# Performance work log

Measured on AMD Instinct MI355X. Metric: run time of the kernel, lower is better.

The kernel has to match this reference:

```python
import jax, jax.numpy as jnp
import numpy as np


def _l2norm(x, axis):
    # F.normalize: x / max(||x||_2, eps)
    n = jnp.sqrt(jnp.sum(x * x, axis=axis, keepdims=True))
    return x / jnp.maximum(n, 1e-12)


def setup_inputs() -> dict:
    key = jax.random.key(0)
    k1, k2 = jax.random.split(key)
    B, N, H = 32768, 2048, 512
    z = jax.random.normal(k1, (B, H), dtype=jnp.float32)
    memory_items = jax.random.normal(k2, (N, H), dtype=jnp.float32)
    return {"z": z, "memory_items": memory_items}


def reference(z, memory_items):
    # ---- read path: cosine-similarity attention over memory bank ----
    z_n = _l2norm(z, axis=1)                     # (B,H)
    m_n = _l2norm(memory_items, axis=1)          # (N,H)
    similarity = z_n @ m_n.T                     # (B,N)
    weights = jax.nn.softmax(similarity, axis=1)  # (B,N)
    z_hat = weights @ memory_items               # (B,H)

    # ---- update path (no-grad in original): vectorized over slots ----
    # row b is "relevant" to slot i iff weights[b,i] >= max_j weights[b,j]
    # (slot i is an argmax for row b). Per-slot softmax over the relevant
    # rows' similarity column, then weighted sum of z -> scatter-add.
    maxw = jnp.max(weights, axis=1, keepdims=True)   # (B,1)
    mask = weights >= maxw                            # (B,N) bool
    neg = jnp.finfo(similarity.dtype).min
    s = jnp.where(mask, similarity, neg)              # (B,N)
    m = jnp.max(s, axis=0)                            # (N,) column max
    p = jnp.where(mask, jnp.exp(s - m), 0.0)          # (B,N)
    denom = jnp.sum(p, axis=0)                        # (N,)
    u = p / jnp.maximum(denom, 1e-30)                 # (B,N) masked softmax per column
    update_term = u.T @ z                             # (N,H)
    count = jnp.sum(mask, axis=0)                     # (N,)
    new_memory = jnp.where(
        (count > 0)[:, None],
        _l2norm(memory_items + update_term, axis=1),
        memory_items,
    )
    return z_hat, new_memory
```

## Files before the change

### kernel.cpp

```cpp
#include <hip/hip_runtime.h>
#include <math.h>

#define B_ROWS 32768
#define N_SLOTS 2048
#define H_DIM 512
#define MCAP 4096

typedef __attribute__((ext_vector_type(8))) _Float16 f16x8;
typedef __attribute__((ext_vector_type(4))) float f32x4;

#define ZPL 132
#define FIX_MARGIN 2.5e-4f
#define XROWS 16

__device__ __forceinline__ unsigned short f2h(float f) {
    union { _Float16 h; unsigned short u; } cv;
    cv.h = (_Float16)f;
    return cv.u;
}
__device__ __forceinline__ unsigned pk2h(float a, float b) {
    return (unsigned)f2h(a) | ((unsigned)f2h(b) << 16);
}
__device__ __forceinline__ unsigned fenc(float f) {
    unsigned b = __float_as_uint(f);
    return (b & 0x80000000u) ? ~b : (b | 0x80000000u);
}

#define STAGE16(g, l) __builtin_amdgcn_global_load_lds( \
    (const __attribute__((address_space(1))) unsigned int*)(g), \
    (__attribute__((address_space(3))) unsigned int*)(l), 16, 0, 0)

#define VWAIT4() asm volatile("s_waitcnt vmcnt(4)" ::: "memory")
#define LWAIT0() asm volatile("s_waitcnt lgkmcnt(0)" ::: "memory")


__global__ __launch_bounds__(256) void prep_z_k(const float* __restrict__ z,
                                                float* __restrict__ zinv,
                                                int* __restrict__ fcnt) {
    if (blockIdx.x == 0 && threadIdx.x == 0) *fcnt = 0;
    int row = blockIdx.x * 4 + (threadIdx.x >> 6);
    int lane = threadIdx.x & 63;
    const float4* p = reinterpret_cast<const float4*>(z + (size_t)row * H_DIM);
    float4 a = p[lane * 2];
    float4 b = p[lane * 2 + 1];
    float s = a.x * a.x + a.y * a.y + a.z * a.z + a.w * a.w
            + b.x * b.x + b.y * b.y + b.z * b.z + b.w * b.w;
#pragma unroll
    for (int m = 32; m >= 1; m >>= 1) s += __shfl_xor(s, m, 64);
    if (lane == 0) zinv[row] = 1.0f / fmaxf(sqrtf(s), 1e-12f);
}

__global__ __launch_bounds__(256) void prep_mem_k(const float* __restrict__ mem,
                                                  float* __restrict__ minv,
                                                  short* __restrict__ mn_sw) {
    int row = blockIdx.x * 4 + (threadIdx.x >> 6);
    int lane = threadIdx.x & 63;
    const float4* p = reinterpret_cast<const float4*>(mem + (size_t)row * H_DIM);
    float4 a = p[lane * 2];
    float4 b = p[lane * 2 + 1];
    float s = a.x * a.x + a.y * a.y + a.z * a.z + a.w * a.w
            + b.x * b.x + b.y * b.y + b.z * b.z + b.w * b.w;
#pragma unroll
    for (int m = 32; m >= 1; m >>= 1) s += __shfl_xor(s, m, 64);
    float inv = 1.0f / fmaxf(sqrtf(s), 1e-12f);
    if (lane == 0) minv[row] = inv;
    uint4 w;
    w.x = pk2h(a.x * inv, a.y * inv);
    w.y = pk2h(a.z * inv, a.w * inv);
    w.z = pk2h(b.x * inv, b.y * inv);
    w.w = pk2h(b.z * inv, b.w * inv);
    char* dst = (char*)mn_sw + ((size_t)row << 10) + ((unsigned)(lane * 16) ^ (unsigned)((row & 7) << 4));
    *reinterpret_cast<uint4*>(dst) = w;
}

__global__ __launch_bounds__(256) void prep_memT_k(const float* __restrict__ mem,
                                                   short* __restrict__ memT_sw) {
    __shared__ short Ts[64][72];
    int bs = blockIdx.x;
    int bh = blockIdx.y;
    int tid = threadIdx.x;
    {
        int s = tid >> 2, c4 = (tid & 3) * 16;
        const float* src = mem + (size_t)(bs * 64 + s) * H_DIM + bh * 64 + c4;
#pragma unroll
        for (int j = 0; j < 4; ++j) {
            float4 v = *reinterpret_cast<const float4*>(src + j * 4);
            Ts[s][c4 + j * 4 + 0] = (short)f2h(v.x);
            Ts[s][c4 + j * 4 + 1] = (short)f2h(v.y);
            Ts[s][c4 + j * 4 + 2] = (short)f2h(v.z);
            Ts[s][c4 + j * 4 + 3] = (short)f2h(v.w);
        }
    }
    __syncthreads();
    int h = tid >> 2, q = tid & 3;
    unsigned w[8];
#pragma unroll
    for (int k = 0; k < 8; ++k) {
        unsigned lo = (unsigned short)Ts[q * 16 + 2 * k][h];
        unsigned hi = (unsigned short)Ts[q * 16 + 2 * k + 1][h];
        w[k] = lo | (hi << 16);
    }
    uint4 c0 = {w[0], w[1], w[2], w[3]};
    uint4 c1 = {w[4], w[5], w[6], w[7]};
    char* dst = (char*)memT_sw + (size_t)(bh * 64 + h) * (N_SLOTS * 2);
    unsigned sw = (unsigned)((h & 7) << 4);
    unsigned b0 = (unsigned)(bs * 128 + q * 32);
    *reinterpret_cast<uint4*>(dst + (b0 ^ sw)) = c0;
    *reinterpret_cast<uint4*>(dst + ((b0 + 16) ^ sw)) = c1;
}


__global__ __launch_bounds__(512, 2) void zhat_k(const float* __restrict__ z,
                                                 const short* __restrict__ mn_sw,
                                                 const short* __restrict__ memT_sw,
                                                 const float* __restrict__ zinv,
                                                 float* __restrict__ rowmax,
                                                 int* __restrict__ rowarg,
                                                 float* __restrict__ rowm2,
                                                 float* __restrict__ out) {
    __shared__ __align__(16) short Mb[4][8192];
    __shared__ __align__(16) short Pl[64 * ZPL];
    __shared__ float pm1[2][64], pm2[2][64], ps[2][64];
    __shared__ int pa1[2][64], pa2[2][64];

    int tid = threadIdx.x;
    int row0 = blockIdx.x * 64;
    int wave = tid >> 6, lane = tid & 63;
    int lm = lane & 15, quad = lane >> 4;
    int rt = wave & 3;
    int wg = wave >> 2;
    int rh = wave & 1;
    int wc = wave >> 1;
    const int swz = (lm & 7) << 4;

#define STAGE_M(buf, c0, kc) do { \
        const char* _g = (const char*)mn_sw + ((size_t)((c0) + wave * 16 + (lane >> 3)) << 10) \
                         + ((kc) << 7) + ((lane & 7) << 4); \
        short* _l = &Mb[buf][wave * 16 * 64]; \
        STAGE16(_g, _l); \
        STAGE16(_g + (8 << 10), _l + 8 * 64); \
    } while (0)

#define STAGE_V(buf, c0, hc) do { \
        const char* _g = (const char*)memT_sw + ((size_t)((hc) * 64 + wave * 8 + (lane >> 4)) << 12) \
                         + ((size_t)(c0) << 1) + ((lane & 15) << 4); \
        short* _l = &Mb[buf][wave * 8 * 128]; \
        STAGE16(_g, _l); \
        STAGE16(_g + (4 << 12), _l + 4 * 128); \
    } while (0)

    STAGE_M(0, 0, 0);
    STAGE_M(1, 0, 1);

    int zrow = row0 + rt * 16 + lm;
    float zi = zinv[zrow];
    f16x8 Zfr[16];
#pragma unroll
    for (int kt = 0; kt < 16; ++kt) {
        const float* zp = z + (size_t)zrow * H_DIM + kt * 32 + quad * 8;
        float4 a = *reinterpret_cast<const float4*>(zp);
        float4 b = *reinterpret_cast<const float4*>(zp + 4);
        union { uint4 u; f16x8 v; } cv;
        cv.u.x = pk2h(a.x * zi, a.y * zi);
        cv.u.y = pk2h(a.z * zi, a.w * zi);
        cv.u.z = pk2h(b.x * zi, b.y * zi);
        cv.u.w = pk2h(b.z * zi, b.w * zi);
        Zfr[kt] = cv.v;
    }

    f32x4 acc[16];
#pragma unroll
    for (int t = 0; t < 16; ++t) acc[t] = (f32x4){0.f, 0.f, 0.f, 0.f};
    float rm1[4], rm2[4], lsum[4];
    int ra1[4], ra2[4];
#pragma unroll
    for (int r = 0; r < 4; ++r) {
        rm1[r] = -3.4e38f; rm2[r] = -3.4e38f; lsum[r] = 0.f; ra1[r] = 0; ra2[r] = 0;
    }

    for (int ct = 0; ct < 16; ++ct) {
        int col0 = ct * 128;
        int col0n = (ct < 15) ? col0 + 128 : 0;
        f32x4 sacc[4];
#pragma unroll
        for (int i = 0; i < 4; ++i) sacc[i] = (f32x4){0.f, 0.f, 0.f, 0.f};

#pragma unroll
        for (int kc = 0; kc < 8; ++kc) {
            if (kc < 6)       STAGE_M((kc + 2) & 3, col0, kc + 2);
            else if (kc == 6) STAGE_V(0, col0, 0);
            else              STAGE_V(1, col0, 1);
            VWAIT4();
            __builtin_amdgcn_s_barrier();
            __builtin_amdgcn_s_setprio(1);
#pragma unroll
            for (int ks = 0; ks < 2; ++ks) {
                f16x8 af = Zfr[kc * 2 + ks];
#pragma unroll
                for (int i = 0; i < 4; ++i) {
                    int srow = (wg * 4 + i) * 16 + lm;
                    int kb = (ks * 64 + quad * 16) ^ swz;
                    f16x8 bfr = *reinterpret_cast<const f16x8*>(
                        (const char*)&Mb[kc & 3][0] + srow * 128 + kb);
                    sacc[i] = __builtin_amdgcn_mfma_f32_16x16x32_f16(af, bfr, sacc[i], 0, 0, 0);
                }
            }
            __builtin_amdgcn_s_setprio(0);
        }

#pragma unroll
        for (int i = 0; i < 4; ++i) {
            int sl = (wg * 4 + i) * 16 + lm;
            int sg = col0 + sl;
#pragma unroll
            for (int r = 0; r < 4; ++r) {
                float v = sacc[i][r];
                if (v > rm1[r]) { rm2[r] = rm1[r]; ra2[r] = ra1[r]; rm1[r] = v; ra1[r] = sg; }
                else if (v > rm2[r]) { rm2[r] = v; ra2[r] = sg; }
                float p = __expf(v);
                lsum[r] += p;
                Pl[(rt * 16 + quad * 4 + r) * ZPL + sl] = (short)f2h(p);
            }
        }
        LWAIT0();
        __builtin_amdgcn_s_barrier();

        f16x8 pa_all[2][4];
#pragma unroll
        for (int rtl = 0; rtl < 2; ++rtl)
#pragma unroll
            for (int ks = 0; ks < 4; ++ks)
                pa_all[rtl][ks] = *reinterpret_cast<const f16x8*>(
                    &Pl[((rh * 2 + rtl) * 16 + lm) * ZPL + ks * 32 + quad * 8]);

#pragma unroll
        for (int hc = 0; hc < 8; ++hc) {
            if (hc < 6)       STAGE_V((hc + 2) & 3, col0, hc + 2);
            else if (hc == 6) STAGE_M(0, col0n, 0);
            else              STAGE_M(1, col0n, 1);
            VWAIT4();
            __builtin_amdgcn_s_barrier();
            __builtin_amdgcn_s_setprio(1);
#pragma unroll
            for (int ks = 0; ks < 4; ++ks) {
                int hl = wc * 16 + lm;
                int kb = (ks * 64 + quad * 16) ^ swz;
                f16x8 vf = *reinterpret_cast<const f16x8*>(
                    (const char*)&Mb[hc & 3][0] + hl * 256 + kb);
                acc[hc * 2 + 0] = __builtin_amdgcn_mfma_f32_16x16x32_f16(pa_all[0][ks], vf, acc[hc * 2 + 0], 0, 0, 0);
                acc[hc * 2 + 1] = __builtin_amdgcn_mfma_f32_16x16x32_f16(pa_all[1][ks], vf, acc[hc * 2 + 1], 0, 0, 0);
            }
            __builtin_amdgcn_s_setprio(0);
        }
    }
    __syncthreads();

#pragma unroll
    for (int mk = 1; mk < 16; mk <<= 1) {
#pragma unroll
        for (int r = 0; r < 4; ++r) {
            float n1 = __shfl_xor(rm1[r], mk, 16);
            int b1 = __shfl_xor(ra1[r], mk, 16);
            float n2 = __shfl_xor(rm2[r], mk, 16);
            int b2 = __shfl_xor(ra2[r], mk, 16);
            if (n1 > rm1[r]) {
                bool c = rm1[r] > n2;
                rm2[r] = c ? rm1[r] : n2; ra2[r] = c ? ra1[r] : b2;
                rm1[r] = n1; ra1[r] = b1;
            } else {
                bool c = n1 > rm2[r];
                rm2[r] = c ? n1 : rm2[r]; ra2[r] = c ? b1 : ra2[r];
            }
            lsum[r] += __shfl_xor(lsum[r], mk, 16);
        }
    }
    if (lm == 0) {
#pragma unroll
        for (int r = 0; r < 4; ++r) {
            int rl = rt * 16 + quad * 4 + r;
            pm1[wg][rl] = rm1[r]; pa1[wg][rl] = ra1[r];
            pm2[wg][rl] = rm2[r]; pa2[wg][rl] = ra2[r];
            ps[wg][rl] = lsum[r];
        }
    }
    __syncthreads();
    if (wave == 0) {
        int r = lane;
        float gm1 = pm1[0][r], gm2 = pm2[0][r];
        int ga1 = pa1[0][r], ga2 = pa2[0][r];
        float n1 = pm1[1][r]; int b1 = pa1[1][r];
        float n2 = pm2[1][r]; int b2 = pa2[1][r];
        if (n1 > gm1) {
            bool c = gm1 > n2;
            gm2 = c ? gm1 : n2; ga2 = c ? ga1 : b2;
            gm1 = n1; ga1 = b1;
        } else {
            bool c = n1 > gm2;
            gm2 = c ? n1 : gm2; ga2 = c ? b1 : ga2;
        }
        rowmax[row0 + r] = gm1; rowarg[row0 + r] = ga1; rowm2[row0 + r] = gm2;
    }
    float linv2[2][4];
#pragma unroll
    for (int rtl = 0; rtl < 2; ++rtl)
#pragma unroll
        for (int r = 0; r < 4; ++r) {
            int rl = (rh * 2 + rtl) * 16 + quad * 4 + r;
            linv2[rtl][r] = 1.0f / (ps[0][rl] + ps[1][rl]);
        }
#pragma unroll
    for (int hc = 0; hc < 8; ++hc)
#pragma unroll
        for (int rtl = 0; rtl < 2; ++rtl) {
            int t = hc * 2 + rtl;
            int h = hc * 64 + wc * 16 + lm;
#pragma unroll
            for (int r = 0; r < 4; ++r) {
                int rg = row0 + (rh * 2 + rtl) * 16 + quad * 4 + r;
                out[(size_t)rg * H_DIM + h] = acc[t][r] * linv2[rtl][r];
            }
        }
}


__global__ __launch_bounds__(256) void flag_k(const float* __restrict__ rowmax,
                                              const float* __restrict__ rowm2,
                                              int* __restrict__ cnt,
                                              int* __restrict__ list,
                                              unsigned long long* __restrict__ packed) {
    int b = blockIdx.x * 256 + threadIdx.x;
    if (rowmax[b] - rowm2[b] < FIX_MARGIN) {
        int p = atomicAdd(cnt, 1);
        list[p] = b;
        packed[p] = 0ull;
    }
}


__global__ __launch_bounds__(256) void exact_k(const float* __restrict__ z,
                                               const float* __restrict__ mem,
                                               const float* __restrict__ minv,
                                               const int* __restrict__ cnt,
                                               const int* __restrict__ list,
                                               unsigned long long* __restrict__ packed) {
    __shared__ float As[32][XROWS + 4];
    __shared__ float Bs[32][132];
    __shared__ int rows[XROWS];
    int tid = threadIdx.x;
    int tx = tid & 15, ty = tid >> 4;
    int n = *cnt;
    int ngroups = (n + XROWS - 1) / XROWS;
    int nunits = ngroups * 16;

    for (int u = blockIdx.x; u < nunits; u += gridDim.x) {
        int g = u >> 4;
        int col0 = (u & 15) * 128;
        __syncthreads();
        if (tid < XROWS) {
            int idx = g * XROWS + tid;
            rows[tid] = list[idx < n ? idx : n - 1];
        }
        __syncthreads();
        float acc[8];
#pragma unroll
        for (int j = 0; j < 8; ++j) acc[j] = 0.f;
        for (int kc = 0; kc < H_DIM; kc += 32) {
            if (tid < 128) {
                int r = tid >> 3, k4 = (tid & 7) * 4;
                float4 v = *reinterpret_cast<const float4*>(z + (size_t)rows[r] * H_DIM + kc + k4);
                As[k4 + 0][r] = v.x;
                As[k4 + 1][r] = v.y;
                As[k4 + 2][r] = v.z;
                As[k4 + 3][r] = v.w;
            }
            int sl = tid >> 1, kq = (tid & 1) * 16;
#pragma unroll
            for (int j = 0; j < 4; ++j) {
                float4 v = *reinterpret_cast<const float4*>(mem + (size_t)(col0 + sl) * H_DIM + kc + kq + j * 4);
                Bs[kq + j * 4 + 0][sl] = v.x;
                Bs[kq + j * 4 + 1][sl] = v.y;
                Bs[kq + j * 4 + 2][sl] = v.z;
                Bs[kq + j * 4 + 3][sl] = v.w;
            }
            __syncthreads();
#pragma unroll 4
            for (int k = 0; k < 32; ++k) {
                float av = As[k][ty];
                const float4 b0 = *reinterpret_cast<const float4*>(&Bs[k][tx * 8]);
                const float4 b1 = *reinterpret_cast<const float4*>(&Bs[k][tx * 8 + 4]);
                acc[0] = fmaf(av, b0.x, acc[0]);
                acc[1] = fmaf(av, b0.y, acc[1]);
                acc[2] = fmaf(av, b0.z, acc[2]);
                acc[3] = fmaf(av, b0.w, acc[3]);
                acc[4] = fmaf(av, b1.x, acc[4]);
                acc[5] = fmaf(av, b1.y, acc[5]);
                acc[6] = fmaf(av, b1.z, acc[6]);
                acc[7] = fmaf(av, b1.w, acc[7]);
            }
            __syncthreads();
        }
        float runM = -3.4e38f;
        int runA = 0;
#pragma unroll
        for (int j = 0; j < 8; ++j) {
            int sg = col0 + tx * 8 + j;
            float s = acc[j] * minv[sg];
            if (s > runM) { runM = s; runA = sg; }
        }
#pragma unroll
        for (int mk = 1; mk < 16; mk <<= 1) {
            float om = __shfl_xor(runM, mk, 16);
            int oa = __shfl_xor(runA, mk, 16);
            if (om > runM || (om == runM && oa < runA)) { runM = om; runA = oa; }
        }
        if (tx == 0) {
            int idx = g * XROWS + ty;
            int tgt = idx < n ? idx : n - 1;
            unsigned long long pk =
                ((unsigned long long)fenc(runM) << 32) | (unsigned)(2047 - runA);
            atomicMax(&packed[tgt], pk);
        }
    }
}

__global__ __launch_bounds__(256) void unpack_k(const int* __restrict__ cnt,
                                                const int* __restrict__ list,
                                                const unsigned long long* __restrict__ packed,
                                                int* __restrict__ rowarg) {
    int p = blockIdx.x * 256 + threadIdx.x;
    if (p < *cnt) {
        int slot = 2047 - (int)(unsigned)(packed[p] & 0xFFFFFFFFull);
        rowarg[list[p]] = slot;
    }
}


__global__ __launch_bounds__(256) void refine_k(const float* __restrict__ z,
                                                const float* __restrict__ mem,
                                                const float* __restrict__ zinv,
                                                const float* __restrict__ minv,
                                                const int* __restrict__ rowarg,
                                                float* __restrict__ rowmax) {
    int row = blockIdx.x * 4 + (threadIdx.x >> 6);
    int lane = threadIdx.x & 63;
    int a = rowarg[row];
    const float4* zp = reinterpret_cast<const float4*>(z + (size_t)row * H_DIM);
    const float4* mp = reinterpret_cast<const float4*>(mem + (size_t)a * H_DIM);
    float d = 0.f;
#pragma unroll
    for (int j = 0; j < 2; ++j) {
        float4 x = zp[lane + j * 64];
        float4 y = mp[lane + j * 64];
        d += x.x * y.x + x.y * y.y + x.z * y.z + x.w * y.w;
    }
#pragma unroll
    for (int m = 32; m >= 1; m >>= 1) d += __shfl_xor(d, m, 64);
    if (lane == 0) rowmax[row] = d * zinv[row] * minv[a];
}


__global__ __launch_bounds__(256) void slot_update_k(const float* __restrict__ mem,
                                                     const float* __restrict__ z,
                                                     const float* __restrict__ rowmax,
                                                     const int* __restrict__ rowarg,
                                                     float* __restrict__ outmem) {
    __shared__ int members[MCAP];
    __shared__ float uval[MCAP];
    __shared__ int cnt;
    __shared__ float red[4];
    __shared__ float bcast;
    int slot = blockIdx.x, tid = threadIdx.x;
    if (tid == 0) cnt = 0;
    __syncthreads();
    for (int b = tid; b < B_ROWS; b += 256) {
        if (rowarg[b] == slot) {
            int p = atomicAdd(&cnt, 1);
            if (p < MCAP) members[p] = b;
        }
    }
    __syncthreads();
    int n = min(cnt, MCAP);
    size_t base = (size_t)slot * H_DIM;
    if (n == 0) {
        for (int h = tid; h < H_DIM; h += 256) outmem[base + h] = mem[base + h];
        return;
    }
    float lm = -3.4e38f;
    for (int j = tid; j < n; j += 256) lm = fmaxf(lm, rowmax[members[j]]);
#pragma unroll
    for (int m = 32; m >= 1; m >>= 1) lm = fmaxf(lm, __shfl_xor(lm, m, 64));
    if ((tid & 63) == 0) red[tid >> 6] = lm;
    __syncthreads();
    if (tid == 0) bcast = fmaxf(fmaxf(red[0], red[1]), fmaxf(red[2], red[3]));
    __syncthreads();
    float mslot = bcast;
    __syncthreads();
    float ls = 0.f;
    for (int j = tid; j < n; j += 256) {
        float u = expf(rowmax[members[j]] - mslot);
        uval[j] = u;
        ls += u;
    }
#pragma unroll
    for (int m = 32; m >= 1; m >>= 1) ls += __shfl_xor(ls, m, 64);
    if ((tid & 63) == 0) red[tid >> 6] = ls;
    __syncthreads();
    if (tid == 0) bcast = (red[0] + red[1]) + (red[2] + red[3]);
    __syncthreads();
    float dinv = 1.0f / fmaxf(bcast, 1e-30f);
    float v0 = mem[base + tid];
    float v1 = mem[base + 256 + tid];
    for (int j = 0; j < n; ++j) {
        float u = uval[j] * dinv;
        size_t zb = (size_t)members[j] * H_DIM;
        v0 = fmaf(u, z[zb + tid], v0);
        v1 = fmaf(u, z[zb + 256 + tid], v1);
    }
    float s = v0 * v0 + v1 * v1;
#pragma unroll
    for (int m = 32; m >= 1; m >>= 1) s += __shfl_xor(s, m, 64);
    if ((tid & 63) == 0) red[tid >> 6] = s;
    __syncthreads();
    if (tid == 0) bcast = (red[0] + red[1]) + (red[2] + red[3]);
    __syncthreads();
    float ninv = 1.0f / fmaxf(sqrtf(bcast), 1e-12f);
    outmem[base + tid] = v0 * ninv;
    outmem[base + 256 + tid] = v1 * ninv;
}


extern "C" void kernel_launch(void* const* d_in, const int* in_sizes, int n_in,
                              void* d_out, int out_size, void* d_ws, size_t ws_size,
                              hipStream_t stream) {
    const float* z = (const float*)d_in[0];
    const float* mem = (const float*)d_in[1];
    float* out_zhat = (float*)d_out;
    float* out_mem = out_zhat + (size_t)B_ROWS * H_DIM;

    char* ws = (char*)d_ws;
    size_t off = 0;
    auto alloc = [&](size_t bytes) -> void* {
        void* p = ws + off;
        off += (bytes + 255) & ~(size_t)255;
        return p;
    };
    float* rowmax = (float*)alloc((size_t)B_ROWS * 4);
    int* rowarg = (int*)alloc((size_t)B_ROWS * 4);
    float* rowm2 = (float*)alloc((size_t)B_ROWS * 4);
    float* zinv = (float*)alloc((size_t)B_ROWS * 4);
    float* minv = (float*)alloc((size_t)N_SLOTS * 4);
    short* mn_sw = (short*)alloc((size_t)N_SLOTS * H_DIM * 2);
    short* memT_sw = (short*)alloc((size_t)H_DIM * N_SLOTS * 2);
    int* fcnt = (int*)alloc(256);
    int* flist = (int*)alloc((size_t)B_ROWS * 4);
    unsigned long long* packed = (unsigned long long*)alloc((size_t)B_ROWS * 8);

    prep_z_k<<<B_ROWS / 4, 256, 0, stream>>>(z, zinv, fcnt);
    prep_mem_k<<<N_SLOTS / 4, 256, 0, stream>>>(mem, minv, mn_sw);
    prep_memT_k<<<dim3(N_SLOTS / 64, H_DIM / 64), 256, 0, stream>>>(mem, memT_sw);
    zhat_k<<<B_ROWS / 64, 512, 0, stream>>>(z, mn_sw, memT_sw, zinv,
                                            rowmax, rowarg, rowm2, out_zhat);
    flag_k<<<B_ROWS / 256, 256, 0, stream>>>(rowmax, rowm2, fcnt, flist, packed);
    exact_k<<<2048, 256, 0, stream>>>(z, mem, minv, fcnt, flist, packed);
    unpack_k<<<B_ROWS / 256, 256, 0, stream>>>(fcnt, flist, packed, rowarg);
    refine_k<<<B_ROWS / 4, 256, 0, stream>>>(z, mem, zinv, minv, rowarg, rowmax);
    slot_update_k<<<N_SLOTS, 256, 0, stream>>>(mem, z, rowmax, rowarg, out_mem);
}
```

Measured before the change: 517.8 us.

## Remap waves to 2x2 row/column tiles in similarity GEMM and drop second-argmax tracking

Changes the wave decomposition of the similarity GEMM so each wave computes two row tiles by two column tiles, matching the layout used by the P@V stage, instead of one row tile by four column tiles. Each LDS B-fragment load now feeds two MFMAs, halving LDS reads for the similarity stage. In exchange each wave keeps two sets of Z fragments in registers, which raises register pressure. It also stops tracking the second-argmax index, simplifies the runner-up merge to fmaxf, and reduces across four waves in the epilogue.

```diff
diff --git a/kernel.cpp b/kernel.cpp
--- a/kernel.cpp
+++ b/kernel.cpp
@@ -120,17 +120,15 @@
                                                  float* __restrict__ out) {
     __shared__ __align__(16) short Mb[4][8192];
     __shared__ __align__(16) short Pl[64 * ZPL];
-    __shared__ float pm1[2][64], pm2[2][64], ps[2][64];
-    __shared__ int pa1[2][64], pa2[2][64];
+    __shared__ float pm1[4][64], pm2[4][64], ps[4][64];
+    __shared__ int pa1[4][64];
 
     int tid = threadIdx.x;
     int row0 = blockIdx.x * 64;
     int wave = tid >> 6, lane = tid & 63;
     int lm = lane & 15, quad = lane >> 4;
-    int rt = wave & 3;
-    int wg = wave >> 2;
-    int rh = wave & 1;
-    int wc = wave >> 1;
+    int rq = wave & 1;
+    int wq = wave >> 1;
     const int swz = (lm & 7) << 4;
 
 #define STAGE_M(buf, c0, kc) do { \
@@ -152,38 +150,46 @@
     STAGE_M(0, 0, 0);
     STAGE_M(1, 0, 1);
 
-    int zrow = row0 + rt * 16 + lm;
-    float zi = zinv[zrow];
-    f16x8 Zfr[16];
-#pragma unroll
-    for (int kt = 0; kt < 16; ++kt) {
-        const float* zp = z + (size_t)zrow * H_DIM + kt * 32 + quad * 8;
-        float4 a = *reinterpret_cast<const float4*>(zp);
-        float4 b = *reinterpret_cast<const float4*>(zp + 4);
-        union { uint4 u; f16x8 v; } cv;
-        cv.u.x = pk2h(a.x * zi, a.y * zi);
-        cv.u.y = pk2h(a.z * zi, a.w * zi);
-        cv.u.z = pk2h(b.x * zi, b.y * zi);
-        cv.u.w = pk2h(b.z * zi, b.w * zi);
-        Zfr[kt] = cv.v;
+    f16x8 Zfr[2][16];
+#pragma unroll
+    for (int rtl = 0; rtl < 2; ++rtl) {
+        int zrow = row0 + (rq * 2 + rtl) * 16 + lm;
+        float zi = zinv[zrow];
+#pragma unroll
+        for (int kt = 0; kt < 16; ++kt) {
+            const float* zp = z + (size_t)zrow * H_DIM + kt * 32 + quad * 8;
+            float4 a = *reinterpret_cast<const float4*>(zp);
+            float4 b = *reinterpret_cast<const float4*>(zp + 4);
+            union { uint4 u; f16x8 v; } cv;
+            cv.u.x = pk2h(a.x * zi, a.y * zi);
+            cv.u.y = pk2h(a.z * zi, a.w * zi);
+            cv.u.z = pk2h(b.x * zi, b.y * zi);
+            cv.u.w = pk2h(b.z * zi, b.w * zi);
+            Zfr[rtl][kt] = cv.v;
+        }
     }
 
     f32x4 acc[16];
 #pragma unroll
     for (int t = 0; t < 16; ++t) acc[t] = (f32x4){0.f, 0.f, 0.f, 0.f};
-    float rm1[4], rm2[4], lsum[4];
-    int ra1[4], ra2[4];
-#pragma unroll
-    for (int r = 0; r < 4; ++r) {
-        rm1[r] = -3.4e38f; rm2[r] = -3.4e38f; lsum[r] = 0.f; ra1[r] = 0; ra2[r] = 0;
-    }
+    float rm1[2][4], rm2[2][4], lsum[2][4];
+    int ra1[2][4];
+#pragma unroll
+    for (int rtl = 0; rtl < 2; ++rtl)
+#pragma unroll
+        for (int r = 0; r < 4; ++r) {
+            rm1[rtl][r] = -3.4e38f; rm2[rtl][r] = -3.4e38f;
+            lsum[rtl][r] = 0.f; ra1[rtl][r] = 0;
+        }
 
     for (int ct = 0; ct < 16; ++ct) {
         int col0 = ct * 128;
         int col0n = (ct < 15) ? col0 + 128 : 0;
-        f32x4 sacc[4];
-#pragma unroll
-        for (int i = 0; i < 4; ++i) sacc[i] = (f32x4){0.f, 0.f, 0.f, 0.f};
+        f32x4 sacc[2][2];
+#pragma unroll
+        for (int rtl = 0; rtl < 2; ++rtl)
+#pragma unroll
+            for (int i = 0; i < 2; ++i) sacc[rtl][i] = (f32x4){0.f, 0.f, 0.f, 0.f};
 
 #pragma unroll
         for (int kc = 0; kc < 8; ++kc) {
@@ -195,33 +201,35 @@
             __builtin_amdgcn_s_setprio(1);
 #pragma unroll
             for (int ks = 0; ks < 2; ++ks) {
-                f16x8 af = Zfr[kc * 2 + ks];
-#pragma unroll
-                for (int i = 0; i < 4; ++i) {
-                    int srow = (wg * 4 + i) * 16 + lm;
+#pragma unroll
+                for (int i = 0; i < 2; ++i) {
+                    int srow = (wq * 2 + i) * 16 + lm;
                     int kb = (ks * 64 + quad * 16) ^ swz;
                     f16x8 bfr = *reinterpret_cast<const f16x8*>(
                         (const char*)&Mb[kc & 3][0] + srow * 128 + kb);
-                    sacc[i] = __builtin_amdgcn_mfma_f32_16x16x32_f16(af, bfr, sacc[i], 0, 0, 0);
+                    sacc[0][i] = __builtin_amdgcn_mfma_f32_16x16x32_f16(Zfr[0][kc * 2 + ks], bfr, sacc[0][i], 0, 0, 0);
+                    sacc[1][i] = __builtin_amdgcn_mfma_f32_16x16x32_f16(Zfr[1][kc * 2 + ks], bfr, sacc[1][i], 0, 0, 0);
                 }
             }
             __builtin_amdgcn_s_setprio(0);
         }
 
 #pragma unroll
-        for (int i = 0; i < 4; ++i) {
-            int sl = (wg * 4 + i) * 16 + lm;
-            int sg = col0 + sl;
-#pragma unroll
-            for (int r = 0; r < 4; ++r) {
-                float v = sacc[i][r];
-                if (v > rm1[r]) { rm2[r] = rm1[r]; ra2[r] = ra1[r]; rm1[r] = v; ra1[r] = sg; }
-                else if (v > rm2[r]) { rm2[r] = v; ra2[r] = sg; }
-                float p = __expf(v);
-                lsum[r] += p;
-                Pl[(rt * 16 + quad * 4 + r) * ZPL + sl] = (short)f2h(p);
-            }
-        }
+        for (int rtl = 0; rtl < 2; ++rtl)
+#pragma unroll
+            for (int i = 0; i < 2; ++i) {
+                int sl = wq * 32 + i * 16 + lm;
+                int sg = col0 + sl;
+#pragma unroll
+                for (int r = 0; r < 4; ++r) {
+                    float v = sacc[rtl][i][r];
+                    if (v > rm1[rtl][r]) { rm2[rtl][r] = rm1[rtl][r]; rm1[rtl][r] = v; ra1[rtl][r] = sg; }
+                    else if (v > rm2[rtl][r]) rm2[rtl][r] = v;
+                    float p = __expf(v);
+                    lsum[rtl][r] += p;
+                    Pl[((rq * 2 + rtl) * 16 + quad * 4 + r) * ZPL + sl] = (short)f2h(p);
+                }
+            }
         LWAIT0();
         __builtin_amdgcn_s_barrier();
 
@@ -231,7 +239,7 @@
 #pragma unroll
             for (int ks = 0; ks < 4; ++ks)
                 pa_all[rtl][ks] = *reinterpret_cast<const f16x8*>(
-                    &Pl[((rh * 2 + rtl) * 16 + lm) * ZPL + ks * 32 + quad * 8]);
+                    &Pl[((rq * 2 + rtl) * 16 + lm) * ZPL + ks * 32 + quad * 8]);
 
 #pragma unroll
         for (int hc = 0; hc < 8; ++hc) {
@@ -243,7 +251,7 @@
             __builtin_amdgcn_s_setprio(1);
 #pragma unroll
             for (int ks = 0; ks < 4; ++ks) {
-                int hl = wc * 16 + lm;
+                int hl = wq * 16 + lm;
                 int kb = (ks * 64 + quad * 16) ^ swz;
                 f16x8 vf = *reinterpret_cast<const f16x8*>(
                     (const char*)&Mb[hc & 3][0] + hl * 256 + kb);
@@ -258,45 +266,42 @@
 #pragma unroll
     for (int mk = 1; mk < 16; mk <<= 1) {
 #pragma unroll
-        for (int r = 0; r < 4; ++r) {
-            float n1 = __shfl_xor(rm1[r], mk, 16);
-            int b1 = __shfl_xor(ra1[r], mk, 16);
-            float n2 = __shfl_xor(rm2[r], mk, 16);
-            int b2 = __shfl_xor(ra2[r], mk, 16);
-            if (n1 > rm1[r]) {
-                bool c = rm1[r] > n2;
-                rm2[r] = c ? rm1[r] : n2; ra2[r] = c ? ra1[r] : b2;
-                rm1[r] = n1; ra1[r] = b1;
-            } else {
-                bool c = n1 > rm2[r];
-                rm2[r] = c ? n1 : rm2[r]; ra2[r] = c ? b1 : ra2[r];
-            }
-            lsum[r] += __shfl_xor(lsum[r], mk, 16);
-        }
+        for (int rtl = 0; rtl < 2; ++rtl)
+#pragma unroll
+            for (int r = 0; r < 4; ++r) {
+                float n1 = __shfl_xor(rm1[rtl][r], mk, 16);
+                int b1 = __shfl_xor(ra1[rtl][r], mk, 16);
+                float n2 = __shfl_xor(rm2[rtl][r], mk, 16);
+                if (n1 > rm1[rtl][r]) {
+                    rm2[rtl][r] = fmaxf(rm1[rtl][r], n2);
+                    rm1[rtl][r] = n1; ra1[rtl][r] = b1;
+                } else {
+                    rm2[rtl][r] = fmaxf(rm2[rtl][r], n1);
+                }
+                lsum[rtl][r] += __shfl_xor(lsum[rtl][r], mk, 16);
+            }
     }
     if (lm == 0) {
 #pragma unroll
-        for (int r = 0; r < 4; ++r) {
-            int rl = rt * 16 + quad * 4 + r;
-            pm1[wg][rl] = rm1[r]; pa1[wg][rl] = ra1[r];
-            pm2[wg][rl] = rm2[r]; pa2[wg][rl] = ra2[r];
-            ps[wg][rl] = lsum[r];
-        }
+        for (int rtl = 0; rtl < 2; ++rtl)
+#pragma unroll
+            for (int r = 0; r < 4; ++r) {
+                int rl = (rq * 2 + rtl) * 16 + quad * 4 + r;
+                pm1[wq][rl] = rm1[rtl][r]; pa1[wq][rl] = ra1[rtl][r];
+                pm2[wq][rl] = rm2[rtl][r]; ps[wq][rl] = lsum[rtl][r];
+            }
     }
     __syncthreads();
     if (wave == 0) {
         int r = lane;
         float gm1 = pm1[0][r], gm2 = pm2[0][r];
-        int ga1 = pa1[0][r], ga2 = pa2[0][r];
-        float n1 = pm1[1][r]; int b1 = pa1[1][r];
-        float n2 = pm2[1][r]; int b2 = pa2[1][r];
-        if (n1 > gm1) {
-            bool c = gm1 > n2;
-            gm2 = c ? gm1 : n2; ga2 = c ? ga1 : b2;
-            gm1 = n1; ga1 = b1;
-        } else {
-            bool c = n1 > gm2;
-            gm2 = c ? n1 : gm2; ga2 = c ? b1 : ga2;
+        int ga1 = pa1[0][r];
+#pragma unroll
+        for (int w2 = 1; w2 < 4; ++w2) {
+            float n1 = pm1[w2][r], n2 = pm2[w2][r];
+            int b1 = pa1[w2][r];
+            if (n1 > gm1) { gm2 = fmaxf(gm1, n2); gm1 = n1; ga1 = b1; }
+            else          { gm2 = fmaxf(gm2, n1); }
         }
         rowmax[row0 + r] = gm1; rowarg[row0 + r] = ga1; rowm2[row0 + r] = gm2;
     }
@@ -305,18 +310,18 @@
     for (int rtl = 0; rtl < 2; ++rtl)
 #pragma unroll
         for (int r = 0; r < 4; ++r) {
-            int rl = (rh * 2 + rtl) * 16 + quad * 4 + r;
-            linv2[rtl][r] = 1.0f / (ps[0][rl] + ps[1][rl]);
+            int rl = (rq * 2 + rtl) * 16 + quad * 4 + r;
+            linv2[rtl][r] = 1.0f / ((ps[0][rl] + ps[1][rl]) + (ps[2][rl] + ps[3][rl]));
         }
 #pragma unroll
     for (int hc = 0; hc < 8; ++hc)
 #pragma unroll
         for (int rtl = 0; rtl < 2; ++rtl) {
             int t = hc * 2 + rtl;
-            int h = hc * 64 + wc * 16 + lm;
+            int h = hc * 64 + wq * 16 + lm;
 #pragma unroll
             for (int r = 0; r < 4; ++r) {
-                int rg = row0 + (rh * 2 + rtl) * 16 + quad * 4 + r;
+                int rg = row0 + (rq * 2 + rtl) * 16 + quad * 4 + r;
                 out[(size_t)rg * H_DIM + h] = acc[t][r] * linv2[rtl][r];
             }
         }
```

New measurement: 629.8 us. 1.22x slower.

## Bucket rows by argmax slot with counting sort instead of per-slot full scans

Applied to the files above, without the earlier changes.

Adds histogram, prefix-scan and scatter kernels that build a compact per-slot member list from rowarg. slot_update_k then reads its members directly instead of every block scanning all rows. It also caches rowmax values in shared memory. This removes the quadratic scan traffic, at the cost of extra small kernel launches and a single-block scan.

```diff
diff --git a/kernel.cpp b/kernel.cpp
--- a/kernel.cpp
+++ b/kernel.cpp
@@ -435,6 +435,52 @@
 }
 
 
+__global__ void zero_counts_k(int* __restrict__ counts) {
+    counts[blockIdx.x * 256 + threadIdx.x] = 0;
+}
+
+__global__ __launch_bounds__(256) void hist_k(const int* __restrict__ rowarg,
+                                              int* __restrict__ counts) {
+    int b = blockIdx.x * 256 + threadIdx.x;
+    atomicAdd(&counts[rowarg[b]], 1);
+}
+
+__global__ __launch_bounds__(256) void scan_k(const int* __restrict__ counts,
+                                              int* __restrict__ offs,
+                                              int* __restrict__ cursor) {
+    __shared__ int s[N_SLOTS];
+    int tid = threadIdx.x;
+    for (int i = tid; i < N_SLOTS; i += 256) s[i] = counts[i];
+    __syncthreads();
+    for (int d = 1; d < N_SLOTS; d <<= 1) {
+        int v[8];
+#pragma unroll
+        for (int k = 0; k < 8; ++k) {
+            int i = tid + k * 256;
+            v[k] = (i >= d) ? s[i - d] : 0;
+        }
+        __syncthreads();
+#pragma unroll
+        for (int k = 0; k < 8; ++k) s[tid + k * 256] += v[k];
+        __syncthreads();
+    }
+    for (int i = tid; i < N_SLOTS; i += 256) {
+        int e = (i == 0) ? 0 : s[i - 1];
+        offs[i] = e;
+        cursor[i] = e;
+    }
+    if (tid == 0) offs[N_SLOTS] = s[N_SLOTS - 1];
+}
+
+__global__ __launch_bounds__(256) void scatter_k(const int* __restrict__ rowarg,
+                                                 int* __restrict__ cursor,
+                                                 int* __restrict__ mlist) {
+    int b = blockIdx.x * 256 + threadIdx.x;
+    int p = atomicAdd(&cursor[rowarg[b]], 1);
+    mlist[p] = b;
+}
+
+
 __global__ __launch_bounds__(256) void refine_k(const float* __restrict__ z,
                                                 const float* __restrict__ mem,
                                                 const float* __restrict__ zinv,
@@ -462,31 +508,29 @@
 __global__ __launch_bounds__(256) void slot_update_k(const float* __restrict__ mem,
                                                      const float* __restrict__ z,
                                                      const float* __restrict__ rowmax,
-                                                     const int* __restrict__ rowarg,
+                                                     const int* __restrict__ offs,
+                                                     const int* __restrict__ mlist,
                                                      float* __restrict__ outmem) {
-    __shared__ int members[MCAP];
+    __shared__ int memb[MCAP];
     __shared__ float uval[MCAP];
-    __shared__ int cnt;
     __shared__ float red[4];
     __shared__ float bcast;
     int slot = blockIdx.x, tid = threadIdx.x;
-    if (tid == 0) cnt = 0;
-    __syncthreads();
-    for (int b = tid; b < B_ROWS; b += 256) {
-        if (rowarg[b] == slot) {
-            int p = atomicAdd(&cnt, 1);
-            if (p < MCAP) members[p] = b;
-        }
-    }
-    __syncthreads();
-    int n = min(cnt, MCAP);
+    int off = offs[slot];
+    int n = min(offs[slot + 1] - off, MCAP);
     size_t base = (size_t)slot * H_DIM;
     if (n == 0) {
         for (int h = tid; h < H_DIM; h += 256) outmem[base + h] = mem[base + h];
         return;
     }
     float lm = -3.4e38f;
-    for (int j = tid; j < n; j += 256) lm = fmaxf(lm, rowmax[members[j]]);
+    for (int j = tid; j < n; j += 256) {
+        int m = mlist[off + j];
+        memb[j] = m;
+        float rm = rowmax[m];
+        uval[j] = rm;
+        lm = fmaxf(lm, rm);
+    }
 #pragma unroll
     for (int m = 32; m >= 1; m >>= 1) lm = fmaxf(lm, __shfl_xor(lm, m, 64));
     if ((tid & 63) == 0) red[tid >> 6] = lm;
@@ -497,7 +541,7 @@
     __syncthreads();
     float ls = 0.f;
     for (int j = tid; j < n; j += 256) {
-        float u = expf(rowmax[members[j]] - mslot);
+        float u = expf(uval[j] - mslot);
         uval[j] = u;
         ls += u;
     }
@@ -512,7 +556,7 @@
     float v1 = mem[base + 256 + tid];
     for (int j = 0; j < n; ++j) {
         float u = uval[j] * dinv;
-        size_t zb = (size_t)members[j] * H_DIM;
+        size_t zb = (size_t)memb[j] * H_DIM;
         v0 = fmaf(u, z[zb + tid], v0);
         v1 = fmaf(u, z[zb + 256 + tid], v1);
     }
@@ -554,15 +598,23 @@
     int* fcnt = (int*)alloc(256);
     int* flist = (int*)alloc((size_t)B_ROWS * 4);
     unsigned long long* packed = (unsigned long long*)alloc((size_t)B_ROWS * 8);
+    int* counts = (int*)alloc((size_t)N_SLOTS * 4);
+    int* offs = (int*)alloc((size_t)(N_SLOTS + 1) * 4);
+    int* cursor = (int*)alloc((size_t)N_SLOTS * 4);
+    int* mlist = (int*)alloc((size_t)B_ROWS * 4);
 
     prep_z_k<<<B_ROWS / 4, 256, 0, stream>>>(z, zinv, fcnt);
     prep_mem_k<<<N_SLOTS / 4, 256, 0, stream>>>(mem, minv, mn_sw);
     prep_memT_k<<<dim3(N_SLOTS / 64, H_DIM / 64), 256, 0, stream>>>(mem, memT_sw);
+    zero_counts_k<<<N_SLOTS / 256, 256, 0, stream>>>(counts);
     zhat_k<<<B_ROWS / 64, 512, 0, stream>>>(z, mn_sw, memT_sw, zinv,
                                             rowmax, rowarg, rowm2, out_zhat);
     flag_k<<<B_ROWS / 256, 256, 0, stream>>>(rowmax, rowm2, fcnt, flist, packed);
     exact_k<<<2048, 256, 0, stream>>>(z, mem, minv, fcnt, flist, packed);
     unpack_k<<<B_ROWS / 256, 256, 0, stream>>>(fcnt, flist, packed, rowarg);
+    hist_k<<<B_ROWS / 256, 256, 0, stream>>>(rowarg, counts);
+    scan_k<<<1, 256, 0, stream>>>(counts, offs, cursor);
+    scatter_k<<<B_ROWS / 256, 256, 0, stream>>>(rowarg, cursor, mlist);
     refine_k<<<B_ROWS / 4, 256, 0, stream>>>(z, mem, zinv, minv, rowarg, rowmax);
-    slot_update_k<<<N_SLOTS, 256, 0, stream>>>(mem, z, rowmax, rowarg, out_mem);
-}
+    slot_update_k<<<N_SLOTS, 256, 0, stream>>>(mem, z, rowmax, offs, mlist, out_mem);
+}
```

After: 479.2 us. 7.5% less time.
